# Performance work log

Hardware: AMD Instinct MI355X
Metric: run time of the kernel (lower is better)

Reference implementation:

```python
import jax, jax.numpy as jnp
import numpy as np


def setup_inputs() -> dict:
    key = jax.random.key(0)
    k1, k2 = jax.random.split(key)
    n, K = 1024, 8
    pred_y = jax.random.normal(k1, (n, K), dtype=jnp.float32)
    true_y = jax.random.randint(k2, (n, K), 0, 2).astype(jnp.int32)  # multi-label 0/1
    return {"pred_y": pred_y, "true_y": true_y}


def reference(pred_y, true_y):
    # mode == 'pairwise2':
    #   sum_{i,j} sum_{a: y[a,i]==1} sum_{b: y[b,j]==0} log(1 + exp(-(pred[a,i] - pred[b,j])))
    #   normalized by |S_pos| * |S_neg| (total counts over the whole label matrix).
    # The double class loop + cartesian_prod is exactly an all-pairs interaction
    # between flattened positive entries and flattened negative entries.
    pos = (true_y == 1)
    neg = (true_y == 0)
    v = pred_y.reshape(-1)                      # [n*K]
    mp = pos.reshape(-1).astype(pred_y.dtype)   # positive-entry mask
    mn = neg.reshape(-1).astype(pred_y.dtype)   # negative-entry mask
    # loss(p - q) = log(1 + exp(-(p - q))) = softplus(q - p)
    diff = v[None, :] - v[:, None]              # [nK, nK]; diff[a, b] = v_b - v_a
    sp = jax.nn.softplus(diff)
    total = jnp.sum(sp * (mp[:, None] * mn[None, :]))
    denom = jnp.sum(mp) * jnp.sum(mn)           # |S_pos| * |S_neg|
    return total / denom
```

## Files before the change

kernel.cpp:

```cpp
#include <hip/hip_runtime.h>

#define CBLK 256
#define PBLK 256
#define PAIR_BLOCKS 2048

__global__ void compact_kernel(const float* __restrict__ v,
                               const int* __restrict__ ty,
                               int* __restrict__ cnt,
                               float* __restrict__ vpos,
                               float* __restrict__ vneg,
                               int N) {
    const int i    = blockIdx.x * blockDim.x + threadIdx.x;
    const int lane = threadIdx.x & 63;

    const bool valid = (i < N);
    float val = 0.0f;
    int   t   = -1;
    if (valid) { val = v[i]; t = ty[i]; }

    const bool isP = valid && (t == 1);
    const bool isN = valid && (t == 0);

    const unsigned long long mp = __ballot(isP);
    const unsigned long long mn = __ballot(isN);
    const unsigned long long lt = (lane == 0) ? 0ull : (~0ull >> (64 - lane));

    int basep = 0, basen = 0;
    if (lane == 0) {
        basep = atomicAdd(&cnt[0], __popcll(mp));
        basen = atomicAdd(&cnt[1], __popcll(mn));
    }
    basep = __shfl(basep, 0, 64);
    basen = __shfl(basen, 0, 64);

    if (isP) vpos[basep + __popcll(mp & lt)] = val;
    if (isN) vneg[basen + __popcll(mn & lt)] = val;
}

__global__ void pair_kernel(const int* __restrict__ cnt,
                            const float* __restrict__ vpos,
                            const float* __restrict__ vneg,
                            float* __restrict__ partials) {
    const int P = cnt[0];
    const int Q = cnt[1];

    float acc = 0.0f;
    for (int b = threadIdx.x; b < Q; b += PBLK) {
        const float vn = vneg[b];
        for (int a = blockIdx.x; a < P; a += gridDim.x) {
            const float x = vn - vpos[a];
            const float e = __expf(-fabsf(x));
            acc += fmaxf(x, 0.0f) + __logf(1.0f + e);
        }
    }

    for (int off = 32; off > 0; off >>= 1)
        acc += __shfl_down(acc, off, 64);

    __shared__ float wsum[PBLK / 64];
    const int lane = threadIdx.x & 63;
    const int wid  = threadIdx.x >> 6;
    if (lane == 0) wsum[wid] = acc;
    __syncthreads();
    if (threadIdx.x == 0) {
        float s = 0.0f;
        #pragma unroll
        for (int w = 0; w < PBLK / 64; ++w) s += wsum[w];
        partials[blockIdx.x] = s;
    }
}

__global__ void finalize_kernel(const float* __restrict__ partials, int nparts,
                                const int* __restrict__ cnt,
                                float* __restrict__ out) {
    const int tid = threadIdx.x;
    double s = 0.0;
    for (int k = tid; k < nparts; k += blockDim.x) s += (double)partials[k];

    __shared__ double sd[256];
    sd[tid] = s;
    __syncthreads();
    for (int off = 128; off > 0; off >>= 1) {
        if (tid < off) sd[tid] += sd[tid + off];
        __syncthreads();
    }
    if (tid == 0) {
        const double denom = (double)cnt[0] * (double)cnt[1];
        out[0] = (float)(sd[0] / denom);
    }
}

extern "C" void kernel_launch(void* const* d_in, const int* in_sizes, int n_in,
                              void* d_out, int out_size, void* d_ws, size_t ws_size,
                              hipStream_t stream) {
    const float* v  = (const float*)d_in[0];
    const int*   ty = (const int*)d_in[1];
    float* out = (float*)d_out;
    const int N = in_sizes[0];

    char*  ws       = (char*)d_ws;
    int*   cnt      = (int*)ws;
    float* vpos     = (float*)(ws + 64);
    float* vneg     = vpos + N;
    float* partials = vneg + N;

    hipMemsetAsync(cnt, 0, 2 * sizeof(int), stream);

    const int cblocks = (N + CBLK - 1) / CBLK;
    compact_kernel<<<cblocks, CBLK, 0, stream>>>(v, ty, cnt, vpos, vneg, N);
    pair_kernel<<<PAIR_BLOCKS, PBLK, 0, stream>>>(cnt, vpos, vneg, partials);
    finalize_kernel<<<1, 256, 0, stream>>>(partials, PAIR_BLOCKS, cnt, out);
}
```

Baseline: 74.14 us.

## Register-tile positives, use base-2 exp/log intrinsics, fuse finalize via last-block ticket

The pair kernel now holds 16 positive values per thread in registers and loops the negatives across blocks, replacing the old per-element global loads inside the inner loop. Inputs are prescaled by log2(e) during compaction so softplus can use the hardware exp2/log2 intrinsics, with a single ln2 factor applied at the end. The separate finalize kernel is removed. The last block to finish, detected with an atomic ticket, sums the partials, which saves a kernel launch. The partials are now summed in float rather than double, and the added instruction-level parallelism may raise register pressure.

```diff
diff --git a/kernel.cpp b/kernel.cpp
--- a/kernel.cpp
+++ b/kernel.cpp
@@ -2,7 +2,26 @@
 
 #define CBLK 256
 #define PBLK 256
-#define PAIR_BLOCKS 2048
+#define GRID 1024
+#define RTILE 16
+
+#define LOG2E 1.4426950408889634f
+#define LN2   0.6931471805599453
+
+__device__ __forceinline__ float fast_exp2(float x) {
+#if __has_builtin(__builtin_amdgcn_exp2f)
+    return __builtin_amdgcn_exp2f(x);
+#else
+    return exp2f(x);
+#endif
+}
+__device__ __forceinline__ float fast_log2(float x) {
+#if __has_builtin(__builtin_amdgcn_logf)
+    return __builtin_amdgcn_logf(x);
+#else
+    return log2f(x);
+#endif
+}
 
 __global__ void compact_kernel(const float* __restrict__ v,
                                const int* __restrict__ ty,
@@ -16,7 +35,7 @@
     const bool valid = (i < N);
     float val = 0.0f;
     int   t   = -1;
-    if (valid) { val = v[i]; t = ty[i]; }
+    if (valid) { val = v[i] * LOG2E; t = ty[i]; }
 
     const bool isP = valid && (t == 1);
     const bool isN = valid && (t == 0);
@@ -37,20 +56,36 @@
     if (isN) vneg[basen + __popcll(mn & lt)] = val;
 }
 
-__global__ void pair_kernel(const int* __restrict__ cnt,
-                            const float* __restrict__ vpos,
-                            const float* __restrict__ vneg,
-                            float* __restrict__ partials) {
-    const int P = cnt[0];
-    const int Q = cnt[1];
+__global__ __launch_bounds__(PBLK) void pair_kernel(
+        const int* __restrict__ cnt,
+        const float* __restrict__ vpos,
+        const float* __restrict__ vneg,
+        float* __restrict__ partials,
+        unsigned int* __restrict__ ticket,
+        float* __restrict__ out) {
+    const int P   = cnt[0];
+    const int Q   = cnt[1];
+    const int tid = threadIdx.x;
 
     float acc = 0.0f;
-    for (int b = threadIdx.x; b < Q; b += PBLK) {
-        const float vn = vneg[b];
-        for (int a = blockIdx.x; a < P; a += gridDim.x) {
-            const float x = vn - vpos[a];
-            const float e = __expf(-fabsf(x));
-            acc += fmaxf(x, 0.0f) + __logf(1.0f + e);
+    for (int base = 0; base < P; base += RTILE * PBLK) {
+        float pv[RTILE], pw[RTILE];
+        #pragma unroll
+        for (int r = 0; r < RTILE; ++r) {
+            const int idx = base + (r << 8) + tid;
+            const bool ok = (idx < P);
+            pv[r] = ok ? vpos[idx] : 0.0f;
+            pw[r] = ok ? 1.0f : 0.0f;
+        }
+        for (int b = blockIdx.x; b < Q; b += GRID) {
+            const float vn = vneg[b];
+            #pragma unroll
+            for (int r = 0; r < RTILE; ++r) {
+                const float x = vn - pv[r];
+                const float e = fast_exp2(-fabsf(x));
+                const float t = fmaxf(x, 0.0f) + fast_log2(1.0f + e);
+                acc = fmaf(pw[r], t, acc);
+            }
         }
     }
 
@@ -58,35 +93,36 @@
         acc += __shfl_down(acc, off, 64);
 
     __shared__ float wsum[PBLK / 64];
-    const int lane = threadIdx.x & 63;
-    const int wid  = threadIdx.x >> 6;
+    __shared__ int lastflag;
+    const int lane = tid & 63;
+    const int wid  = tid >> 6;
     if (lane == 0) wsum[wid] = acc;
     __syncthreads();
-    if (threadIdx.x == 0) {
+    if (tid == 0) {
         float s = 0.0f;
         #pragma unroll
         for (int w = 0; w < PBLK / 64; ++w) s += wsum[w];
         partials[blockIdx.x] = s;
+        __threadfence();
+        const unsigned int t = atomicAdd(ticket, 1u);
+        lastflag = (t == GRID - 1) ? 1 : 0;
     }
-}
+    __syncthreads();
 
-__global__ void finalize_kernel(const float* __restrict__ partials, int nparts,
-                                const int* __restrict__ cnt,
-                                float* __restrict__ out) {
-    const int tid = threadIdx.x;
-    double s = 0.0;
-    for (int k = tid; k < nparts; k += blockDim.x) s += (double)partials[k];
-
-    __shared__ double sd[256];
-    sd[tid] = s;
-    __syncthreads();
-    for (int off = 128; off > 0; off >>= 1) {
-        if (tid < off) sd[tid] += sd[tid + off];
+    if (lastflag) {
+        __threadfence();
+        float s = 0.0f;
+        for (int k = tid; k < GRID; k += PBLK) s += partials[k];
+        for (int off = 32; off > 0; off >>= 1)
+            s += __shfl_down(s, off, 64);
+        if (lane == 0) wsum[wid] = s;
         __syncthreads();
-    }
-    if (tid == 0) {
-        const double denom = (double)cnt[0] * (double)cnt[1];
-        out[0] = (float)(sd[0] / denom);
+        if (tid == 0) {
+            double tot = 0.0;
+            #pragma unroll
+            for (int w = 0; w < PBLK / 64; ++w) tot += (double)wsum[w];
+            out[0] = (float)(tot * LN2 / ((double)P * (double)Q));
+        }
     }
 }
 
@@ -100,14 +136,14 @@
 
     char*  ws       = (char*)d_ws;
     int*   cnt      = (int*)ws;
+    unsigned int* ticket = (unsigned int*)(ws + 8);
     float* vpos     = (float*)(ws + 64);
     float* vneg     = vpos + N;
     float* partials = vneg + N;
 
-    hipMemsetAsync(cnt, 0, 2 * sizeof(int), stream);
+    hipMemsetAsync(ws, 0, 16, stream);
 
     const int cblocks = (N + CBLK - 1) / CBLK;
     compact_kernel<<<cblocks, CBLK, 0, stream>>>(v, ty, cnt, vpos, vneg, N);
-    pair_kernel<<<PAIR_BLOCKS, PBLK, 0, stream>>>(cnt, vpos, vneg, partials);
-    finalize_kernel<<<1, 256, 0, stream>>>(partials, PAIR_BLOCKS, cnt, out);
+    pair_kernel<<<GRID, PBLK, 0, stream>>>(cnt, vpos, vneg, partials, ticket, out);
 }
```

New measurement: 85.05 us. +14.7%, slower.
